# Performance work log

Measured on AMD Instinct MI355X. Metric: run time of the kernel, lower is better.

Reference implementation:

```python
import jax, jax.numpy as jnp
import numpy as np

B, S, H, DH, HQ, HKV = 2, 1024, 2048, 128, 16, 4
E, K, I, IS = 16, 4, 1024, 1024
EPS = 1e-5
ROPE_BASE = 10000.0
ROUTED_SCALE = 1.0


def rmsnorm(x, w):
    v = jnp.mean(x.astype(jnp.float32) ** 2, axis=-1, keepdims=True)
    return (x.astype(jnp.float32) * jax.lax.rsqrt(v + EPS)).astype(x.dtype) * w


def rope(x, cos, sin):
    x1, x2 = jnp.split(x, 2, axis=-1)
    return jnp.concatenate([x1 * cos - x2 * sin, x2 * cos + x1 * sin], axis=-1)


def setup_inputs() -> dict:
    key = jax.random.key(0)
    ks = jax.random.split(key, 24)
    s = 0.02
    inp = {}
    inp['x'] = jax.random.normal(ks[0], (B, S, H), dtype=jnp.float32)
    inp['in_ln_w'] = jnp.ones((H,), jnp.float32)
    inp['wq'] = jax.random.normal(ks[1], (H, HQ * DH), jnp.float32) * s
    inp['bq'] = jax.random.normal(ks[2], (HQ * DH,), jnp.float32) * s
    inp['wk'] = jax.random.normal(ks[3], (H, HKV * DH), jnp.float32) * s
    inp['bk'] = jax.random.normal(ks[4], (HKV * DH,), jnp.float32) * s
    inp['wv'] = jax.random.normal(ks[5], (H, HKV * DH), jnp.float32) * s
    inp['bv'] = jax.random.normal(ks[6], (HKV * DH,), jnp.float32) * s
    inp['qn_w'] = jnp.ones((DH,), jnp.float32)
    inp['kn_w'] = jnp.ones((DH,), jnp.float32)
    inp['wo'] = jax.random.normal(ks[7], (HQ * DH, H), jnp.float32) * s
    inp['post_ln_w'] = jnp.ones((H,), jnp.float32)
    inp['gate_w'] = jax.random.normal(ks[8], (E, H), jnp.float32) * s
    inp['gate_b'] = jax.random.normal(ks[9], (E,), jnp.float32) * s
    inp['wg'] = jax.random.normal(ks[10], (E, H, I), jnp.float32) * s
    inp['wu'] = jax.random.normal(ks[11], (E, H, I), jnp.float32) * s
    inp['wd'] = jax.random.normal(ks[12], (E, I, H), jnp.float32) * s
    inp['swg'] = jax.random.normal(ks[13], (H, IS), jnp.float32) * s
    inp['swu'] = jax.random.normal(ks[14], (H, IS), jnp.float32) * s
    inp['swd'] = jax.random.normal(ks[15], (IS, H), jnp.float32) * s
    return inp


def reference(x, in_ln_w, wq, bq, wk, bk, wv, bv, qn_w, kn_w, wo, post_ln_w,
              gate_w, gate_b, wg, wu, wd, swg, swu, swd):
    # ---- attention block ----
    res = x
    h = rmsnorm(x, in_ln_w)
    q = (h @ wq + bq).reshape(B, S, HQ, DH)
    k = (h @ wk + bk).reshape(B, S, HKV, DH)
    v = (h @ wv + bv).reshape(B, S, HKV, DH)
    q = rmsnorm(q, qn_w)  # per-head QK norm over head_dim
    k = rmsnorm(k, kn_w)
    inv_freq = 1.0 / (ROPE_BASE ** (jnp.arange(0, DH, 2, dtype=jnp.float32) / DH))  # [DH/2]
    fr = jnp.arange(S, dtype=jnp.float32)[:, None] * inv_freq[None, :]  # [S, DH/2]
    cos = jnp.cos(fr)[None, :, None, :]
    sin = jnp.sin(fr)[None, :, None, :]
    q = rope(q, cos, sin)
    k = rope(k, cos, sin)
    g = HQ // HKV
    k = jnp.repeat(k, g, axis=2)  # GQA expand to [B,S,HQ,DH]
    v = jnp.repeat(v, g, axis=2)
    scores = jnp.einsum('bqhd,bkhd->bhqk', q, k) * (DH ** -0.5)
    causal = jnp.tril(jnp.ones((S, S), dtype=bool))
    scores = jnp.where(causal[None, None], scores, jnp.float32(-1e30))
    attn = jax.nn.softmax(scores, axis=-1)
    o = jnp.einsum('bhqk,bkhd->bqhd', attn, v).reshape(B, S, HQ * DH) @ wo
    x = res + o
    # ---- MoE block ----
    res = x
    h = rmsnorm(x, post_ln_w)
    ht = h.reshape(B * S, H)  # [T, H]
    logits = ht.astype(jnp.float32) @ gate_w.T  # fp32 router
    scr = jax.nn.sigmoid(logits)  # [T, E]
    choice = scr + gate_b[None, :]  # noaux_tc: bias only for selection
    _, topi = jax.lax.top_k(choice, K)  # [T, K]
    tw = jnp.take_along_axis(scr, topi, axis=-1)  # unbiased combine weights
    tw = tw / (jnp.sum(tw, axis=-1, keepdims=True) + 1e-20)  # norm_topk_prob
    tw = tw * ROUTED_SCALE
    cw = jnp.sum(jax.nn.one_hot(topi, E, dtype=jnp.float32) * tw[..., None], axis=1)  # [T, E]
    a = jnp.einsum('th,ehi->eti', ht, wg)
    b = jnp.einsum('th,ehi->eti', ht, wu)
    inter = jax.nn.silu(a) * b * cw.T[:, :, None]  # scale before down-proj
    routed = jnp.einsum('eti,eih->th', inter, wd)
    shared = (jax.nn.silu(ht @ swg) * (ht @ swu)) @ swd
    out = res + (routed + shared).reshape(B, S, H)
    return out
```

## Files before the change

### kernel.cpp

```cpp
#include <hip/hip_runtime.h>
#include <math.h>

typedef unsigned short u16;
typedef __attribute__((ext_vector_type(8))) short short8;
typedef __attribute__((ext_vector_type(4))) float f32x4;

#define B_ 2
#define S_ 1024
#define H_ 2048
#define DH_ 128
#define HQ_ 16
#define HKV_ 4
#define E_ 16
#define TOPK_ 4
#define I_ 1024
#define T_ (B_*S_)
#define NQKV_ 3072
#define NSEG_ 17
#define NA_ (T_*TOPK_ + T_)
#define K3_ 6144
#define MAXTILE 97

#define QPLANE ((long)B_*HQ_*S_*DH_)
#define KPLANE ((long)B_*HKV_*S_*DH_)
#define VPLANE ((long)B_*HKV_*DH_*S_)

__device__ __forceinline__ float bf2f(u16 u){
  union { unsigned int i; float f; } x; x.i = ((unsigned int)u) << 16; return x.f;
}
__device__ __forceinline__ u16 f2bf(float f){
  union { float f; unsigned int i; } x; x.f = f;
  unsigned int r = x.i + 0x7fffu + ((x.i >> 16) & 1u);
  return (u16)(r >> 16);
}
__device__ __forceinline__ void split_bf(float v, u16& hi, u16& lo){
  hi = f2bf(v);
  lo = f2bf(v - bf2f(hi));
}

__device__ __forceinline__ void gld_lds16(const void* g, void* l){
  __builtin_amdgcn_global_load_lds(
      (const __attribute__((address_space(1))) unsigned int*)g,
      (__attribute__((address_space(3))) unsigned int*)l, 16, 0, 0);
}

__device__ __forceinline__ f32x4 mfma_bf16(short8 a, short8 b, f32x4 c){
  return __builtin_amdgcn_mfma_f32_16x16x32_bf16(a, b, c, 0, 0, 0);
}

__global__ void k_transpose(const float* __restrict__ in, u16* __restrict__ out,
                            int R, int C, int rowMul, int rowOff,
                            long inBatch, long outBatch, int split3)
{
  __shared__ float tile[32][33];
  const float* inp = in + (long)blockIdx.z * inBatch;
  u16* outp = out + (long)blockIdx.z * outBatch;
  int c0 = blockIdx.x * 32, r0 = blockIdx.y * 32;
  int tx = threadIdx.x, ty = threadIdx.y;
#pragma unroll
  for (int i = 0; i < 4; i++)
    tile[ty*4+i][tx] = inp[(long)(r0 + ty*4 + i) * C + c0 + tx];
  __syncthreads();
#pragma unroll
  for (int i = 0; i < 4; i++){
    int c = c0 + ty*4 + i;
    float v = tile[tx][ty*4+i];
    if (split3){
      u16 hi, lo; split_bf(v, hi, lo);
      long base = (long)(c*rowMul + rowOff) * (3*R);
      outp[base + r0 + tx]       = hi;
      outp[base + R + r0 + tx]   = lo;
      outp[base + 2*R + r0 + tx] = hi;
    } else {
      outp[(long)(c*rowMul + rowOff) * R + r0 + tx] = f2bf(v);
    }
  }
}

__global__ void k_rmsnorm(const float* __restrict__ x, const float* __restrict__ w,
                          u16* __restrict__ out3)
{
  int t = blockIdx.x;
  const float4* r4 = (const float4*)(x + (long)t * H_);
  const float4* w4 = (const float4*)w;
  float4 a = r4[threadIdx.x], b = r4[threadIdx.x + 256];
  float ss = a.x*a.x + a.y*a.y + a.z*a.z + a.w*a.w
           + b.x*b.x + b.y*b.y + b.z*b.z + b.w*b.w;
#pragma unroll
  for (int d = 1; d < 64; d <<= 1) ss += __shfl_xor(ss, d);
  __shared__ float red[4];
  int lane = threadIdx.x & 63, wv = threadIdx.x >> 6;
  if (lane == 0) red[wv] = ss;
  __syncthreads();
  ss = red[0] + red[1] + red[2] + red[3];
  float rs = rsqrtf(ss * (1.f / 2048.f) + 1e-5f);
  float4 wa = w4[threadIdx.x], wb = w4[threadIdx.x + 256];
  float va[8] = { a.x*rs*wa.x, a.y*rs*wa.y, a.z*rs*wa.z, a.w*rs*wa.w,
                  b.x*rs*wb.x, b.y*rs*wb.y, b.z*rs*wb.z, b.w*rs*wb.w };
  int pos0 = threadIdx.x*4, pos1 = 1024 + threadIdx.x*4;
  ushort4 hi0, lo0, hi1, lo1;
  split_bf(va[0], hi0.x, lo0.x); split_bf(va[1], hi0.y, lo0.y);
  split_bf(va[2], hi0.z, lo0.z); split_bf(va[3], hi0.w, lo0.w);
  split_bf(va[4], hi1.x, lo1.x); split_bf(va[5], hi1.y, lo1.y);
  split_bf(va[6], hi1.z, lo1.z); split_bf(va[7], hi1.w, lo1.w);
  u16* row = out3 + (long)t * K3_;
  *(ushort4*)(row + pos0) = hi0;        *(ushort4*)(row + pos1) = hi1;
  *(ushort4*)(row + 2048 + pos0) = hi0; *(ushort4*)(row + 2048 + pos1) = hi1;
  *(ushort4*)(row + 4096 + pos0) = lo0; *(ushort4*)(row + 4096 + pos1) = lo1;
}

__global__ void k_add_rmsnorm(const float* __restrict__ x, const float* __restrict__ p0,
                              const float* __restrict__ w, float* __restrict__ xa,
                              u16* __restrict__ out1, float* __restrict__ outf)
{
  int t = blockIdx.x;
  long base = (long)t * H_;
  const float4* x4 = (const float4*)(x + base);
  const float4* a4 = (const float4*)(p0 + base);
  const float4* w4 = (const float4*)w;
  int i0 = threadIdx.x, i1 = threadIdx.x + 256;
  float4 xv0 = x4[i0], xv1 = x4[i1];
  float4 av0 = a4[i0], av1 = a4[i1];
  float4 s0, s1;
  s0.x = xv0.x+av0.x; s0.y = xv0.y+av0.y; s0.z = xv0.z+av0.z; s0.w = xv0.w+av0.w;
  s1.x = xv1.x+av1.x; s1.y = xv1.y+av1.y; s1.z = xv1.z+av1.z; s1.w = xv1.w+av1.w;
  *(float4*)(xa + base + i0*4) = s0;
  *(float4*)(xa + base + i1*4) = s1;
  float ss = s0.x*s0.x + s0.y*s0.y + s0.z*s0.z + s0.w*s0.w
           + s1.x*s1.x + s1.y*s1.y + s1.z*s1.z + s1.w*s1.w;
#pragma unroll
  for (int d = 1; d < 64; d <<= 1) ss += __shfl_xor(ss, d);
  __shared__ float red[4];
  int lane = threadIdx.x & 63, wv = threadIdx.x >> 6;
  if (lane == 0) red[wv] = ss;
  __syncthreads();
  ss = red[0] + red[1] + red[2] + red[3];
  float rs = rsqrtf(ss * (1.f / 2048.f) + 1e-5f);
  float4 wa = w4[i0], wb = w4[i1];
  float va[8] = { s0.x*rs*wa.x, s0.y*rs*wa.y, s0.z*rs*wa.z, s0.w*rs*wa.w,
                  s1.x*rs*wb.x, s1.y*rs*wb.y, s1.z*rs*wb.z, s1.w*rs*wb.w };
  ushort4 q0 = { f2bf(va[0]), f2bf(va[1]), f2bf(va[2]), f2bf(va[3]) };
  ushort4 q1 = { f2bf(va[4]), f2bf(va[5]), f2bf(va[6]), f2bf(va[7]) };
  *(ushort4*)(out1 + base + i0*4) = q0;
  *(ushort4*)(out1 + base + i1*4) = q1;
  float4 oa = { va[0], va[1], va[2], va[3] };
  float4 ob = { va[4], va[5], va[6], va[7] };
  *(float4*)(outf + base + i0*4) = oa;
  *(float4*)(outf + base + i1*4) = ob;
}

__global__ void k_ropetab(float* __restrict__ tab){
  int s = blockIdx.x, i = threadIdx.x;
  double inv = pow(10000.0, -(double)i / 64.0);
  double fr = (double)s * inv;
  tab[s*128 + i]      = (float)cos(fr);
  tab[s*128 + 64 + i] = (float)sin(fr);
}

__global__ void k_ropenorm(const float* __restrict__ qkv, const float* __restrict__ biascat,
                           const float* __restrict__ qnw, const float* __restrict__ knw,
                           const float* __restrict__ tab,
                           u16* __restrict__ Q, u16* __restrict__ Kn, u16* __restrict__ Vt)
{
  long gw = (long)blockIdx.x * 4 + (threadIdx.x >> 6);
  int lane = threadIdx.x & 63;
  int hr = (int)(gw % 24);
  long bs = gw / 24;
  int s = (int)(bs % S_);
  int b = (int)(bs / S_);
  long ro = bs * NQKV_ + hr * DH_;
  float x1 = qkv[ro + lane] + biascat[hr*DH_ + lane];
  float x2 = qkv[ro + lane + 64] + biascat[hr*DH_ + lane + 64];
  if (hr < 20){
    float ss = x1*x1 + x2*x2;
#pragma unroll
    for (int d = 1; d < 64; d <<= 1) ss += __shfl_xor(ss, d);
    float rs = rsqrtf(ss * (1.f/128.f) + 1e-5f);
    const float* wn = (hr < 16) ? qnw : knw;
    float y1 = x1 * rs * wn[lane], y2 = x2 * rs * wn[lane + 64];
    float c = tab[s*128 + lane], sn = tab[s*128 + 64 + lane];
    float o1 = y1*c - y2*sn, o2 = y2*c + y1*sn;
    if (hr < 16){
      const float sc = 0.088388347648318447f;
      u16 h1,l1,h2,l2;
      split_bf(o1*sc, h1, l1); split_bf(o2*sc, h2, l2);
      u16* dst = Q + (((long)b*HQ_ + hr)*S_ + s) * DH_;
      dst[lane] = h1; dst[lane+64] = h2;
      dst[QPLANE + lane] = l1; dst[QPLANE + lane+64] = l2;
    } else {
      u16 h1,l1,h2,l2;
      split_bf(o1, h1, l1); split_bf(o2, h2, l2);
      u16* dst = Kn + (((long)b*HKV_ + (hr-16))*S_ + s) * DH_;
      dst[lane] = h1; dst[lane+64] = h2;
      dst[KPLANE + lane] = l1; dst[KPLANE + lane+64] = l2;
    }
  } else {
    u16 h1,l1,h2,l2;
    split_bf(x1, h1, l1); split_bf(x2, h2, l2);
    u16* dst = Vt + (((long)b*HKV_ + (hr-20))*DH_) * S_ + s;
    dst[(long)lane * S_]        = h1;
    dst[(long)(lane + 64) * S_] = h2;
    dst[VPLANE + (long)lane * S_]        = l1;
    dst[VPLANE + (long)(lane + 64) * S_] = l2;
  }
}

__launch_bounds__(256)
__global__ void k_attn(const u16* __restrict__ Q, const u16* __restrict__ Kn,
                       const u16* __restrict__ Vt, u16* __restrict__ O3)
{
  __shared__ u16 Ksh[32][128];
  __shared__ u16 Ksl[32][128];
  __shared__ u16 Vsh[128][32];
  __shared__ u16 Vsl[128][32];
  __shared__ u16 Psh[4][16][40];
  __shared__ u16 Psl[4][16][40];
  int qb = blockIdx.x, h = blockIdx.y, b = blockIdx.z;
  int kvh = h >> 2;
  int q0 = qb * 64;
  int tid = threadIdx.x, lane = tid & 63, w = tid >> 6;

  const u16* Qg = Q  + (((long)b*HQ_  + h  )*S_ + q0) * DH_;
  const u16* Kg = Kn + (((long)b*HKV_ + kvh)*S_) * DH_;
  const u16* Vg = Vt + (((long)b*HKV_ + kvh)*DH_) * S_;

  short8 qh[4], ql[4];
  {
    long qrow = w*16 + (lane & 15);
    int coff = (lane >> 4) << 3;
#pragma unroll
    for (int kst = 0; kst < 4; kst++){
      qh[kst] = *(const short8*)(Qg + qrow*DH_ + kst*32 + coff);
      ql[kst] = *(const short8*)(Qg + QPLANE + qrow*DH_ + kst*32 + coff);
    }
  }

  f32x4 o[8];
#pragma unroll
  for (int nt = 0; nt < 8; nt++) o[nt] = (f32x4){0.f,0.f,0.f,0.f};
  float mrow[4] = {-INFINITY,-INFINITY,-INFINITY,-INFINITY};
  float lrow[4] = {0.f,0.f,0.f,0.f};

  for (int j = 0; j <= 2*qb + 1; ++j){
#pragma unroll
    for (int it = 0; it < 2; ++it){
      int flat = it*256 + tid;
      int r = flat >> 4, pc = flat & 15;
      int c = pc ^ (((r&7) << 1) | ((r >> 3) & 1));
      long gsrc = ((long)(j*32 + r))*DH_ + c*8;
      gld_lds16(Kg + gsrc,          &Ksh[0][0] + (it*256 + (w<<6))*8);
      gld_lds16(Kg + KPLANE + gsrc, &Ksl[0][0] + (it*256 + (w<<6))*8);
    }
#pragma unroll
    for (int it = 0; it < 2; ++it){
      int flat = it*256 + tid;
      int r = flat >> 2, pc = flat & 3;
      int c = pc ^ (r & 3);
      long gsrc = (long)r*S_ + j*32 + c*8;
      gld_lds16(Vg + gsrc,          &Vsh[0][0] + (it*256 + (w<<6))*8);
      gld_lds16(Vg + VPLANE + gsrc, &Vsl[0][0] + (it*256 + (w<<6))*8);
    }
    __syncthreads();

    f32x4 s[2];
#pragma unroll
    for (int nt = 0; nt < 2; nt++) s[nt] = (f32x4){0.f,0.f,0.f,0.f};
#pragma unroll
    for (int kst = 0; kst < 4; kst++){
#pragma unroll
      for (int nt = 0; nt < 2; nt++){
        int br = nt*16 + (lane & 15);
        int bc = (kst*4 + (lane >> 4)) ^ (((br&7)<<1) | ((br>>3)&1));
        short8 kh = *(const short8*)&Ksh[br][bc*8];
        short8 kl = *(const short8*)&Ksl[br][bc*8];
        s[nt] = mfma_bf16(qh[kst], kh, s[nt]);
        s[nt] = mfma_bf16(qh[kst], kl, s[nt]);
        s[nt] = mfma_bf16(ql[kst], kh, s[nt]);
      }
    }
    if (j >= 2*qb){
#pragma unroll
      for (int nt = 0; nt < 2; nt++){
        int key = j*32 + nt*16 + (lane & 15);
#pragma unroll
        for (int r = 0; r < 4; r++){
          int qrow = q0 + w*16 + ((lane >> 4) << 2) + r;
          if (key > qrow) s[nt][r] = -1e30f;
        }
      }
    }
    float pm[4];
#pragma unroll
    for (int r = 0; r < 4; r++) pm[r] = fmaxf(s[0][r], s[1][r]);
#pragma unroll
    for (int d = 1; d < 16; d <<= 1){
#pragma unroll
      for (int r = 0; r < 4; r++) pm[r] = fmaxf(pm[r], __shfl_xor(pm[r], d));
    }
    float alpha[4];
#pragma unroll
    for (int r = 0; r < 4; r++){
      float mn = fmaxf(mrow[r], pm[r]);
      alpha[r] = __expf(mrow[r] - mn);
      mrow[r] = mn;
    }
    float psum[4] = {0.f,0.f,0.f,0.f};
#pragma unroll
    for (int nt = 0; nt < 2; nt++){
#pragma unroll
      for (int r = 0; r < 4; r++){
        float p = __expf(s[nt][r] - mrow[r]);
        psum[r] += p;
        u16 ph, pl; split_bf(p, ph, pl);
        int qr = ((lane>>4)<<2) + r, kc = nt*16 + (lane & 15);
        Psh[w][qr][kc] = ph;
        Psl[w][qr][kc] = pl;
      }
    }
#pragma unroll
    for (int d = 1; d < 16; d <<= 1){
#pragma unroll
      for (int r = 0; r < 4; r++) psum[r] += __shfl_xor(psum[r], d);
    }
#pragma unroll
    for (int r = 0; r < 4; r++) lrow[r] = lrow[r]*alpha[r] + psum[r];
#pragma unroll
    for (int nt = 0; nt < 8; nt++)
#pragma unroll
      for (int r = 0; r < 4; r++) o[nt][r] *= alpha[r];

    {
      short8 pah = *(const short8*)&Psh[w][lane & 15][(lane >> 4) << 3];
      short8 pal = *(const short8*)&Psl[w][lane & 15][(lane >> 4) << 3];
#pragma unroll
      for (int nt = 0; nt < 8; nt++){
        int br = nt*16 + (lane & 15);
        int bc = (lane >> 4) ^ (br & 3);
        short8 vh = *(const short8*)&Vsh[br][bc*8];
        short8 vl = *(const short8*)&Vsl[br][bc*8];
        o[nt] = mfma_bf16(pah, vh, o[nt]);
        o[nt] = mfma_bf16(pah, vl, o[nt]);
        o[nt] = mfma_bf16(pal, vh, o[nt]);
      }
    }
    __syncthreads();
  }
  float inv_[4];
#pragma unroll
  for (int r = 0; r < 4; r++) inv_[r] = 1.f / lrow[r];
#pragma unroll
  for (int nt = 0; nt < 8; nt++){
#pragma unroll
    for (int r = 0; r < 4; r++){
      long row = (long)b*S_ + q0 + w*16 + ((lane >> 4) << 2) + r;
      float val = o[nt][r] * inv_[r];
      u16 hi, lo; split_bf(val, hi, lo);
      long base = row*K3_ + h*DH_ + nt*16 + (lane & 15);
      O3[base]        = hi;
      O3[base + 2048] = hi;
      O3[base + 4096] = lo;
    }
  }
}

template<int MODE, int KITERS>
__launch_bounds__(256)
__global__ void k_gemm(const u16* __restrict__ A, const u16* __restrict__ Bm,
                       void* __restrict__ Cout,
                       int N, int Kstride, long segStrideB,
                       const int* __restrict__ segStart, const int* __restrict__ segCount,
                       const int* __restrict__ tileSeg, const int* __restrict__ tileMb,
                       const int* __restrict__ meta,
                       const int* __restrict__ assignTS, const float* __restrict__ assignW,
                       u16* __restrict__ downb)
{
  __shared__ u16 LDS[4*8192];
  int tid = threadIdx.x;
  int lane = tid & 63, w = tid >> 6;
  int wr = w >> 1, wc = w & 1;
  int n0 = blockIdx.x * 128;
  int seg = 0, m0, segBase = 0, cnt = 1 << 30;
  if constexpr (MODE >= 2){
    int ty = blockIdx.y;
    if (ty >= meta[0]) return;
    seg = tileSeg[ty]; m0 = tileMb[ty] * 128;
    segBase = segStart[seg];
    cnt = segCount[seg];
  } else {
    m0 = blockIdx.y * 128;
  }
  const u16* Bp = Bm + (long)seg * segStrideB;

  const u16* aS[2]; const u16* bS[2];
#pragma unroll
  for (int it = 0; it < 2; ++it){
    int c = w + it*4;
    int row = c*16 + (lane >> 2);
    int ps = (lane & 3) ^ ((row >> 1) & 3);
    long arow;
    if constexpr (MODE == 2) arow = (long)(assignTS[segBase + m0 + row] >> 3);
    else if constexpr (MODE == 3) arow = (long)(segBase + m0 + row);
    else arow = (long)(m0 + row);
    aS[it] = A + arow * Kstride + ps*8;
    bS[it] = Bp + (long)(n0 + row) * Kstride + ps*8;
  }

  int offA[4], offB[4];
#pragma unroll
  for (int m = 0; m < 4; m++){
    int r = wr*64 + m*16 + (lane & 15);
    int ps = (lane >> 4) ^ ((r >> 1) & 3);
    offA[m] = r*32 + ps*8;
  }
#pragma unroll
  for (int n = 0; n < 4; n++){
    int r = wc*64 + n*16 + (lane & 15);
    int ps = (lane >> 4) ^ ((r >> 1) & 3);
    offB[n] = 4096 + r*32 + ps*8;
  }

  f32x4 acc[4][4];
#pragma unroll
  for (int m = 0; m < 4; m++)
#pragma unroll
    for (int n = 0; n < 4; n++) acc[m][n] = (f32x4){0.f,0.f,0.f,0.f};

  auto STAGE = [&](int Tt){
    int kb = Tt * 32;
    int db = (Tt & 3) * 8192;
#pragma unroll
    for (int it = 0; it < 2; ++it){
      gld_lds16(aS[it] + kb, &LDS[db + (w + it*4)*512]);
      gld_lds16(bS[it] + kb, &LDS[db + 4096 + (w + it*4)*512]);
    }
  };

  STAGE(0); STAGE(1); STAGE(2);

  for (int T = 0; T < KITERS; ++T){
    if (T + 3 < KITERS) STAGE(T + 3);
    int rem = KITERS - 1 - T;
    if (rem >= 3)      asm volatile("s_waitcnt vmcnt(12)" ::: "memory");
    else if (rem == 2) asm volatile("s_waitcnt vmcnt(8)"  ::: "memory");
    else if (rem == 1) asm volatile("s_waitcnt vmcnt(4)"  ::: "memory");
    else               asm volatile("s_waitcnt vmcnt(0)"  ::: "memory");
    __builtin_amdgcn_s_barrier();
    __builtin_amdgcn_sched_barrier(0);
    const u16* L = &LDS[(T & 3) * 8192];
    short8 af[4], bfv[4];
#pragma unroll
    for (int m = 0; m < 4; m++) af[m]  = *(const short8*)(L + offA[m]);
#pragma unroll
    for (int n = 0; n < 4; n++) bfv[n] = *(const short8*)(L + offB[n]);
#pragma unroll
    for (int m = 0; m < 4; m++)
#pragma unroll
      for (int n = 0; n < 4; n++)
        acc[m][n] = mfma_bf16(af[m], bfv[n], acc[m][n]);
    asm volatile("s_waitcnt lgkmcnt(0)" ::: "memory");
    __builtin_amdgcn_sched_barrier(0);
    __builtin_amdgcn_s_barrier();
  }

  if constexpr (MODE == 0){
    float* C = (float*)Cout;
#pragma unroll
    for (int m = 0; m < 4; m++){
      int row0 = m0 + wr*64 + m*16 + ((lane >> 4) << 2);
#pragma unroll
      for (int n = 0; n < 4; n++){
        int col = n0 + wc*64 + n*16 + (lane & 15);
#pragma unroll
        for (int r = 0; r < 4; r++)
          C[(long)(row0 + r)*N + col] = acc[m][n][r];
      }
    }
  } else if constexpr (MODE == 2){
    u16* inter = (u16*)Cout;
#pragma unroll
    for (int m = 0; m < 4; m++){
      int row0 = m0 + wr*64 + m*16 + ((lane >> 4) << 2);
#pragma unroll
      for (int n = 0; n < 4; n++){
        f32x4 a = acc[m][n];
        float ov[4];
#pragma unroll
        for (int r = 0; r < 4; r++) ov[r] = __shfl_xor(a[r], 1);
        if ((lane & 1) == 0){
          int colp = (n0 + wc*64 + n*16 + (lane & 15)) >> 1;
#pragma unroll
          for (int r = 0; r < 4; r++){
            int rl = row0 + r;
            if (rl < cnt){
              int pos = segBase + rl;
              float g = a[r], u = ov[r];
              float val = (g / (1.f + __expf(-g))) * u * assignW[pos];
              inter[(long)pos*I_ + colp] = f2bf(val);
            }
          }
        }
      }
    }
  } else {
#pragma unroll
    for (int m = 0; m < 4; m++){
      int row0 = m0 + wr*64 + m*16 + ((lane >> 4) << 2);
#pragma unroll
      for (int n = 0; n < 4; n++){
        int col = n0 + wc*64 + n*16 + (lane & 15);
#pragma unroll
        for (int r = 0; r < 4; r++){
          int rl = row0 + r;
          if (rl < cnt){
            int ts = assignTS[segBase + rl];
            downb[((long)(ts >> 3)*5 + (ts & 7))*H_ + col] = f2bf(acc[m][n][r]);
          }
        }
      }
    }
  }
}

__global__ void k_router(const float* __restrict__ ht, const float* __restrict__ gw,
                         const float* __restrict__ gb, int* __restrict__ tok_e,
                         float* __restrict__ tok_w, int* __restrict__ counts)
{
  int t = blockIdx.x * 4 + (threadIdx.x >> 6);
  int lane = threadIdx.x & 63;
  const float4* row4 = (const float4*)(ht + (long)t * H_);
  float acc[16];
#pragma unroll
  for (int e = 0; e < 16; e++) acc[e] = 0.f;
#pragma unroll
  for (int it = 0; it < 8; it++){
    float4 rv = row4[lane + 64*it];
#pragma unroll
    for (int e = 0; e < 16; e++){
      float4 gv = *(const float4*)(gw + (long)e*H_ + (lane + 64*it)*4);
      acc[e] += rv.x*gv.x + rv.y*gv.y + rv.z*gv.z + rv.w*gv.w;
    }
  }
#pragma unroll
  for (int d = 1; d < 64; d <<= 1){
#pragma unroll
    for (int e = 0; e < 16; e++) acc[e] += __shfl_xor(acc[e], d);
  }
  if (lane == 0){
    float scr[16], ch[16];
#pragma unroll
    for (int e = 0; e < 16; e++){
      float s = 1.f / (1.f + __expf(-acc[e]));
      scr[e] = s; ch[e] = s + gb[e];
    }
    int sel[4]; float tw[4]; float sum = 0.f;
#pragma unroll
    for (int k = 0; k < 4; k++){
      int best = -1; float bv = -1e30f;
      for (int e = 0; e < 16; e++){
        bool used = false;
        for (int j = 0; j < k; j++) if (sel[j] == e) used = true;
        if (!used && ch[e] > bv){ bv = ch[e]; best = e; }
      }
      sel[k] = best; tw[k] = scr[best]; sum += scr[best];
    }
    float inv = 1.f / (sum + 1e-20f);
#pragma unroll
    for (int k = 0; k < 4; k++){
      tok_e[t*4 + k] = sel[k];
      tok_w[t*4 + k] = tw[k] * inv;
      atomicAdd(&counts[sel[k]], 1);
    }
  }
}

__global__ void k_scan(const int* __restrict__ counts, int* __restrict__ segStart,
                       int* __restrict__ segCount, int* __restrict__ cursor,
                       int* __restrict__ tileSeg, int* __restrict__ tileMb,
                       int* __restrict__ meta)
{
  if (threadIdx.x == 0){
    int off = 0, nt = 0;
    for (int e = 0; e < 16; e++){
      segStart[e] = off; segCount[e] = counts[e]; cursor[e] = off;
      for (int mb = 0; mb*128 < counts[e]; ++mb){ tileSeg[nt] = e; tileMb[nt] = mb; nt++; }
      off += counts[e];
    }
    segStart[16] = T_*TOPK_; segCount[16] = T_;
    for (int mb = 0; mb < 16; ++mb){ tileSeg[nt] = 16; tileMb[nt] = mb; nt++; }
    meta[0] = nt;
  }
}

__global__ void k_scatter(const int* __restrict__ tok_e, const float* __restrict__ tok_w,
                          int* __restrict__ cursor, int* __restrict__ assignTS,
                          float* __restrict__ assignW)
{
  int t = blockIdx.x*256 + threadIdx.x;
  if (t < T_){
    for (int k = 0; k < 4; k++){
      int e = tok_e[t*4 + k];
      int pos = atomicAdd(&cursor[e], 1);
      assignTS[pos] = t*8 + k;
      assignW[pos] = tok_w[t*4 + k];
    }
    assignTS[T_*TOPK_ + t] = t*8 + 4;
    assignW[T_*TOPK_ + t] = 1.f;
  }
}

__global__ void k_final(const float* __restrict__ xa, const u16* __restrict__ downb,
                        float* __restrict__ out)
{
  long i = ((long)blockIdx.x*256 + threadIdx.x) * 4;
  int t = (int)(i >> 11);
  int h = (int)(i & 2047);
  float4 r = *(const float4*)(xa + i);
  float a0 = r.x, a1 = r.y, a2 = r.z, a3 = r.w;
#pragma unroll
  for (int k = 0; k < 5; k++){
    const u16* d = downb + ((long)t*5 + k)*H_ + h;
    ushort4 v = *(const ushort4*)d;
    a0 += bf2f(v.x); a1 += bf2f(v.y); a2 += bf2f(v.z); a3 += bf2f(v.w);
  }
  float4 o = { a0, a1, a2, a3 };
  *(float4*)(out + i) = o;
}

extern "C" void kernel_launch(void* const* d_in, const int* in_sizes, int n_in,
                              void* d_out, int out_size, void* d_ws, size_t ws_size,
                              hipStream_t stream)
{
  (void)in_sizes; (void)n_in; (void)out_size; (void)ws_size;
  const float* x      = (const float*)d_in[0];
  const float* inlnw  = (const float*)d_in[1];
  const float* wq     = (const float*)d_in[2];
  const float* bq     = (const float*)d_in[3];
  const float* wk     = (const float*)d_in[4];
  const float* bk     = (const float*)d_in[5];
  const float* wv     = (const float*)d_in[6];
  const float* bv     = (const float*)d_in[7];
  const float* qnw    = (const float*)d_in[8];
  const float* knw    = (const float*)d_in[9];
  const float* wo     = (const float*)d_in[10];
  const float* postln = (const float*)d_in[11];
  const float* gatew  = (const float*)d_in[12];
  const float* gateb  = (const float*)d_in[13];
  const float* wg     = (const float*)d_in[14];
  const float* wu     = (const float*)d_in[15];
  const float* wdp    = (const float*)d_in[16];
  const float* swg    = (const float*)d_in[17];
  const float* swu    = (const float*)d_in[18];
  const float* swd    = (const float*)d_in[19];
  float* out = (float*)d_out;

  char* ws = (char*)d_ws;
  size_t off = 0;
  auto alloc = [&](size_t bytes) -> char* {
    char* p = ws + off; off += (bytes + 255) & ~(size_t)255; return p;
  };
  u16*   wqkv2   = (u16*)  alloc((size_t)NQKV_*K3_*2);
  u16*   wo2     = (u16*)  alloc((size_t)H_*K3_*2);
  u16*   wgu_t   = (u16*)  alloc((size_t)NSEG_*2048*2048*2);
  u16*   wd_t    = (u16*)  alloc((size_t)NSEG_*2048*1024*2);
  float* tab     = (float*)alloc((size_t)S_*128*4);
  float* biascat = (float*)alloc((size_t)NQKV_*4);
  float* xa      = (float*)alloc((size_t)T_*H_*4);
  int*   tok_e   = (int*)  alloc((size_t)T_*4*4);
  float* tok_w   = (float*)alloc((size_t)T_*4*4);
  int*   counts  = (int*)  alloc(32*4);
  int*   segStart= (int*)  alloc(32*4);
  int*   segCount= (int*)  alloc(32*4);
  int*   cursor  = (int*)  alloc(32*4);
  int*   tileSeg = (int*)  alloc(128*4);
  int*   tileMb  = (int*)  alloc(128*4);
  int*   meta    = (int*)  alloc(32*4);
  int*   assignTS= (int*)  alloc((size_t)NA_*4);
  float* assignW = (float*)alloc((size_t)NA_*4);
  char*  scrA    = alloc((size_t)T_*K3_*2);
  char*  scrBC   = alloc((size_t)2*T_*NQKV_*4);
  char*  scrD    = alloc((size_t)(2*QPLANE + 2*KPLANE + 2*VPLANE)*2);

  u16*   h2      = (u16*)scrA;
  u16*   attno2  = (u16*)scrA;
  u16*   inter   = (u16*)scrA;
  float* qkvp0   = (float*)scrBC;
  float* wop     = (float*)scrBC;
  u16*   Qb2     = (u16*)scrD;
  u16*   Kn2     = (u16*)(scrD + (size_t)2*QPLANE*2);
  u16*   Vt2     = (u16*)(scrD + (size_t)2*QPLANE*2 + (size_t)2*KPLANE*2);
  float* ht_f    = (float*)scrD;
  u16*   ht_b    = (u16*)(scrD + (size_t)T_*H_*4);
  u16*   downb   = (u16*)scrD;

  dim3 tb(32, 8);
  k_transpose<<<dim3(64,64,1),  tb, 0, stream>>>(wq,  wqkv2, 2048, 2048, 1, 0,    0, 0, 1);
  k_transpose<<<dim3(16,64,1),  tb, 0, stream>>>(wk,  wqkv2, 2048, 512,  1, 2048, 0, 0, 1);
  k_transpose<<<dim3(16,64,1),  tb, 0, stream>>>(wv,  wqkv2, 2048, 512,  1, 2560, 0, 0, 1);
  k_transpose<<<dim3(64,64,1),  tb, 0, stream>>>(wo,  wo2,   2048, 2048, 1, 0,    0, 0, 1);
  k_transpose<<<dim3(32,64,16), tb, 0, stream>>>(wg,  wgu_t, 2048, 1024, 2, 0, (long)2048*1024, (long)2048*2048, 0);
  k_transpose<<<dim3(32,64,16), tb, 0, stream>>>(wu,  wgu_t, 2048, 1024, 2, 1, (long)2048*1024, (long)2048*2048, 0);
  k_transpose<<<dim3(32,64,1),  tb, 0, stream>>>(swg, wgu_t + (long)16*2048*2048, 2048, 1024, 2, 0, 0, 0, 0);
  k_transpose<<<dim3(32,64,1),  tb, 0, stream>>>(swu, wgu_t + (long)16*2048*2048, 2048, 1024, 2, 1, 0, 0, 0);
  k_transpose<<<dim3(64,32,16), tb, 0, stream>>>(wdp, wd_t,  1024, 2048, 1, 0, (long)1024*2048, (long)2048*1024, 0);
  k_transpose<<<dim3(64,32,1),  tb, 0, stream>>>(swd, wd_t + (long)16*2048*1024, 1024, 2048, 1, 0, 0, 0, 0);

  hipMemcpyAsync(biascat,        bq, 2048*4, hipMemcpyDeviceToDevice, stream);
  hipMemcpyAsync(biascat + 2048, bk, 512*4,  hipMemcpyDeviceToDevice, stream);
  hipMemcpyAsync(biascat + 2560, bv, 512*4,  hipMemcpyDeviceToDevice, stream);

  k_ropetab<<<S_, 64, 0, stream>>>(tab);
  k_rmsnorm<<<T_, 256, 0, stream>>>(x, inlnw, h2);

  k_gemm<0,192><<<dim3(24,16), 256, 0, stream>>>(h2, wqkv2, qkvp0,
      NQKV_, K3_, 0, nullptr, nullptr, nullptr, nullptr, nullptr, nullptr, nullptr, nullptr);

  k_ropenorm<<<(T_*24)/4, 256, 0, stream>>>(qkvp0, biascat, qnw, knw, tab, Qb2, Kn2, Vt2);

  k_attn<<<dim3(S_/64, HQ_, B_), 256, 0, stream>>>(Qb2, Kn2, Vt2, attno2);

  k_gemm<0,192><<<dim3(16,16), 256, 0, stream>>>(attno2, wo2, wop,
      H_, K3_, 0, nullptr, nullptr, nullptr, nullptr, nullptr, nullptr, nullptr, nullptr);

  k_add_rmsnorm<<<T_, 256, 0, stream>>>(x, wop, postln, xa, ht_b, ht_f);

  hipMemsetAsync(counts, 0, 32*4, stream);
  k_router<<<T_/4, 256, 0, stream>>>(ht_f, gatew, gateb, tok_e, tok_w, counts);
  k_scan<<<1, 64, 0, stream>>>(counts, segStart, segCount, cursor, tileSeg, tileMb, meta);
  k_scatter<<<(T_+255)/256, 256, 0, stream>>>(tok_e, tok_w, cursor, assignTS, assignW);

  k_gemm<2,64><<<dim3(16,MAXTILE), 256, 0, stream>>>(ht_b, wgu_t, inter,
      2048, H_, (long)2048*2048, segStart, segCount, tileSeg, tileMb, meta, assignTS, assignW, nullptr);

  k_gemm<3,32><<<dim3(16,MAXTILE), 256, 0, stream>>>(inter, wd_t, nullptr,
      H_, I_, (long)2048*1024, segStart, segCount, tileSeg, tileMb, meta, assignTS, assignW, downb);

  k_final<<<(T_*H_/4)/256, 256, 0, stream>>>(xa, downb, out);
}
```

Baseline: 899.8 us.

## Give MoE grouped GEMMs a BK=64 single-buffer kernel separate from dense GEMM

Splits the shared templated GEMM into a dense kernel (unchanged 4-stage pipeline, K-tile 32) and a new grouped MoE kernel. The MoE kernel uses a K-tile of 64 with XOR-swizzled 128x64 LDS tiles and two MFMA sub-steps per load. It gives up the multi-stage pipelined prefetch in favour of fewer, larger loads and fewer barriers per K element. The risk is that load latency is no longer hidden across stages, since each iteration waits on its own global-to-LDS copy.

After: 858.1 us. 1.05x faster.

```diff
diff --git a/kernel.cpp b/kernel.cpp
--- a/kernel.cpp
+++ b/kernel.cpp
@@ -363,33 +363,17 @@
   }
 }
 
-template<int MODE, int KITERS>
+template<int KITERS>
 __launch_bounds__(256)
-__global__ void k_gemm(const u16* __restrict__ A, const u16* __restrict__ Bm,
-                       void* __restrict__ Cout,
-                       int N, int Kstride, long segStrideB,
-                       const int* __restrict__ segStart, const int* __restrict__ segCount,
-                       const int* __restrict__ tileSeg, const int* __restrict__ tileMb,
-                       const int* __restrict__ meta,
-                       const int* __restrict__ assignTS, const float* __restrict__ assignW,
-                       u16* __restrict__ downb)
+__global__ void k_gemm_d(const u16* __restrict__ A, const u16* __restrict__ Bm,
+                         float* __restrict__ C, int N, int Kstride)
 {
   __shared__ u16 LDS[4*8192];
   int tid = threadIdx.x;
   int lane = tid & 63, w = tid >> 6;
   int wr = w >> 1, wc = w & 1;
   int n0 = blockIdx.x * 128;
-  int seg = 0, m0, segBase = 0, cnt = 1 << 30;
-  if constexpr (MODE >= 2){
-    int ty = blockIdx.y;
-    if (ty >= meta[0]) return;
-    seg = tileSeg[ty]; m0 = tileMb[ty] * 128;
-    segBase = segStart[seg];
-    cnt = segCount[seg];
-  } else {
-    m0 = blockIdx.y * 128;
-  }
-  const u16* Bp = Bm + (long)seg * segStrideB;
+  int m0 = blockIdx.y * 128;
 
   const u16* aS[2]; const u16* bS[2];
 #pragma unroll
@@ -397,12 +381,8 @@
     int c = w + it*4;
     int row = c*16 + (lane >> 2);
     int ps = (lane & 3) ^ ((row >> 1) & 3);
-    long arow;
-    if constexpr (MODE == 2) arow = (long)(assignTS[segBase + m0 + row] >> 3);
-    else if constexpr (MODE == 3) arow = (long)(segBase + m0 + row);
-    else arow = (long)(m0 + row);
-    aS[it] = A + arow * Kstride + ps*8;
-    bS[it] = Bp + (long)(n0 + row) * Kstride + ps*8;
+    aS[it] = A + (long)(m0 + row) * Kstride + ps*8;
+    bS[it] = Bm + (long)(n0 + row) * Kstride + ps*8;
   }
 
   int offA[4], offB[4];
@@ -462,20 +442,95 @@
     __builtin_amdgcn_s_barrier();
   }
 
-  if constexpr (MODE == 0){
-    float* C = (float*)Cout;
-#pragma unroll
-    for (int m = 0; m < 4; m++){
-      int row0 = m0 + wr*64 + m*16 + ((lane >> 4) << 2);
+#pragma unroll
+  for (int m = 0; m < 4; m++){
+    int row0 = m0 + wr*64 + m*16 + ((lane >> 4) << 2);
+#pragma unroll
+    for (int n = 0; n < 4; n++){
+      int col = n0 + wc*64 + n*16 + (lane & 15);
+#pragma unroll
+      for (int r = 0; r < 4; r++)
+        C[(long)(row0 + r)*N + col] = acc[m][n][r];
+    }
+  }
+}
+
+template<int MODE>
+__launch_bounds__(256)
+__global__ void k_gemm_g(const u16* __restrict__ A, const u16* __restrict__ Bm,
+                         void* __restrict__ Cout,
+                         int Kloop, long segStrideB,
+                         const int* __restrict__ segStart, const int* __restrict__ segCount,
+                         const int* __restrict__ tileSeg, const int* __restrict__ tileMb,
+                         const int* __restrict__ meta,
+                         const int* __restrict__ assignTS, const float* __restrict__ assignW,
+                         u16* __restrict__ downb)
+{
+  __shared__ u16 As[128][64];
+  __shared__ u16 Bs[128][64];
+  int tid = threadIdx.x;
+  int lane = tid & 63, w = tid >> 6;
+  int wr = w >> 1, wc = w & 1;
+  int n0 = blockIdx.x * 128;
+  int ty = blockIdx.y;
+  if (ty >= meta[0]) return;
+  int seg = tileSeg[ty], m0 = tileMb[ty] * 128;
+  int segBase = segStart[seg];
+  int cnt = segCount[seg];
+  const u16* Bp = Bm + (long)seg * segStrideB;
+
+  const u16* aS[4]; const u16* bS[4];
+#pragma unroll
+  for (int it = 0; it < 4; ++it){
+    int flat = it*256 + tid;
+    int r = flat >> 3, pc = flat & 7;
+    int c = pc ^ (r & 7);
+    long arow;
+    if constexpr (MODE == 2) arow = (long)(assignTS[segBase + m0 + r] >> 3);
+    else arow = (long)(segBase + m0 + r);
+    aS[it] = A + arow * Kloop + c*8;
+    bS[it] = Bp + (long)(n0 + r) * Kloop + c*8;
+  }
+
+  f32x4 acc[4][4];
+#pragma unroll
+  for (int m = 0; m < 4; m++)
+#pragma unroll
+    for (int n = 0; n < 4; n++) acc[m][n] = (f32x4){0.f,0.f,0.f,0.f};
+
+  u16* AsF = &As[0][0]; u16* BsF = &Bs[0][0];
+  for (int k0 = 0; k0 < Kloop; k0 += 64){
+#pragma unroll
+    for (int it = 0; it < 4; ++it){
+      gld_lds16(aS[it] + k0, AsF + (it*256 + (w<<6))*8);
+      gld_lds16(bS[it] + k0, BsF + (it*256 + (w<<6))*8);
+    }
+    __syncthreads();
+#pragma unroll
+    for (int kh = 0; kh < 2; ++kh){
+      short8 af[4], bfv[4];
+#pragma unroll
+      for (int m = 0; m < 4; m++){
+        int r = wr*64 + m*16 + (lane & 15);
+        int c = (kh*4 + (lane >> 4)) ^ (r & 7);
+        af[m] = *(const short8*)&As[r][c*8];
+      }
 #pragma unroll
       for (int n = 0; n < 4; n++){
-        int col = n0 + wc*64 + n*16 + (lane & 15);
-#pragma unroll
-        for (int r = 0; r < 4; r++)
-          C[(long)(row0 + r)*N + col] = acc[m][n][r];
-      }
-    }
-  } else if constexpr (MODE == 2){
+        int r = wc*64 + n*16 + (lane & 15);
+        int c = (kh*4 + (lane >> 4)) ^ (r & 7);
+        bfv[n] = *(const short8*)&Bs[r][c*8];
+      }
+#pragma unroll
+      for (int m = 0; m < 4; m++)
+#pragma unroll
+        for (int n = 0; n < 4; n++)
+          acc[m][n] = mfma_bf16(af[m], bfv[n], acc[m][n]);
+    }
+    __syncthreads();
+  }
+
+  if constexpr (MODE == 2){
     u16* inter = (u16*)Cout;
 #pragma unroll
     for (int m = 0; m < 4; m++){
@@ -711,15 +766,13 @@
   k_ropetab<<<S_, 64, 0, stream>>>(tab);
   k_rmsnorm<<<T_, 256, 0, stream>>>(x, inlnw, h2);
 
-  k_gemm<0,192><<<dim3(24,16), 256, 0, stream>>>(h2, wqkv2, qkvp0,
-      NQKV_, K3_, 0, nullptr, nullptr, nullptr, nullptr, nullptr, nullptr, nullptr, nullptr);
+  k_gemm_d<192><<<dim3(24,16), 256, 0, stream>>>(h2, wqkv2, qkvp0, NQKV_, K3_);
 
   k_ropenorm<<<(T_*24)/4, 256, 0, stream>>>(qkvp0, biascat, qnw, knw, tab, Qb2, Kn2, Vt2);
 
   k_attn<<<dim3(S_/64, HQ_, B_), 256, 0, stream>>>(Qb2, Kn2, Vt2, attno2);
 
-  k_gemm<0,192><<<dim3(16,16), 256, 0, stream>>>(attno2, wo2, wop,
-      H_, K3_, 0, nullptr, nullptr, nullptr, nullptr, nullptr, nullptr, nullptr, nullptr);
+  k_gemm_d<192><<<dim3(16,16), 256, 0, stream>>>(attno2, wo2, wop, H_, K3_);
 
   k_add_rmsnorm<<<T_, 256, 0, stream>>>(x, wop, postln, xa, ht_b, ht_f);
 
@@ -728,11 +781,11 @@
   k_scan<<<1, 64, 0, stream>>>(counts, segStart, segCount, cursor, tileSeg, tileMb, meta);
   k_scatter<<<(T_+255)/256, 256, 0, stream>>>(tok_e, tok_w, cursor, assignTS, assignW);
 
-  k_gemm<2,64><<<dim3(16,MAXTILE), 256, 0, stream>>>(ht_b, wgu_t, inter,
-      2048, H_, (long)2048*2048, segStart, segCount, tileSeg, tileMb, meta, assignTS, assignW, nullptr);
-
-  k_gemm<3,32><<<dim3(16,MAXTILE), 256, 0, stream>>>(inter, wd_t, nullptr,
-      H_, I_, (long)2048*1024, segStart, segCount, tileSeg, tileMb, meta, assignTS, assignW, downb);
+  k_gemm_g<2><<<dim3(16,MAXTILE), 256, 0, stream>>>(ht_b, wgu_t, inter,
+      H_, (long)2048*2048, segStart, segCount, tileSeg, tileMb, meta, assignTS, assignW, nullptr);
+
+  k_gemm_g<3><<<dim3(16,MAXTILE), 256, 0, stream>>>(inter, wd_t, nullptr,
+      I_, (long)2048*1024, segStart, segCount, tileSeg, tileMb, meta, assignTS, assignW, downb);
 
   k_final<<<(T_*H_/4)/256, 256, 0, stream>>>(xa, downb, out);
 }
```
